# Kernel tuning notes

Measured on AMD Instinct MI355X. Metric: run time of the kernel, lower is better.

The kernel has to match this reference:

```python
import jax, jax.numpy as jnp
import numpy as np

EPS = 1e-5


def setup_inputs() -> dict:
    key = jax.random.key(0)
    ks = jax.random.split(key, 10)
    B, C, H, W = 8, 128, 64, 64
    inputs = jax.random.normal(ks[0], (B, C, H, W), dtype=jnp.float32)
    # GroupNorm affine params
    gn_w = jnp.ones((C,), dtype=jnp.float32)
    gn_b = jnp.zeros((C,), dtype=jnp.float32)
    # Linear layers: torch nn.Linear weight is [out, in]
    s = 1.0 / np.sqrt(C)
    Wq = jax.random.uniform(ks[1], (C, C), jnp.float32, -s, s)
    bq = jax.random.uniform(ks[2], (C,), jnp.float32, -s, s)
    Wk = jax.random.uniform(ks[3], (C, C), jnp.float32, -s, s)
    bk = jax.random.uniform(ks[4], (C,), jnp.float32, -s, s)
    Wv = jax.random.uniform(ks[5], (C, C), jnp.float32, -s, s)
    bv = jax.random.uniform(ks[6], (C,), jnp.float32, -s, s)
    Wp = jax.random.uniform(ks[7], (C, C), jnp.float32, -s, s)
    bp = jax.random.uniform(ks[8], (C,), jnp.float32, -s, s)
    return {"inputs": inputs, "gn_w": gn_w, "gn_b": gn_b,
            "Wq": Wq, "bq": bq, "Wk": Wk, "bk": bk,
            "Wv": Wv, "bv": bv, "Wp": Wp, "bp": bp,
            "groups": 32}


def _group_norm(x, w, b, groups):
    B, C, H, W = x.shape
    xg = x.reshape(B, groups, C // groups, H, W)
    mu = jnp.mean(xg, axis=(2, 3, 4), keepdims=True)
    var = jnp.var(xg, axis=(2, 3, 4), keepdims=True)
    xn = ((xg - mu) * jax.lax.rsqrt(var + EPS)).reshape(B, C, H, W)
    return xn * w[None, :, None, None] + b[None, :, None, None]


def reference(inputs, gn_w, gn_b, Wq, bq, Wk, bk, Wv, bv, Wp, bp, groups):
    B, C, H, W = inputs.shape
    scale = C ** (-0.5)
    normed = _group_norm(inputs, gn_w, gn_b, groups)  # [B,C,H,W]
    x = normed.transpose(0, 2, 3, 1).reshape(B, H * W, C)  # [B,N,C] tokens
    q = x @ Wq.T + bq
    k = x @ Wk.T + bk
    v = x @ Wv.T + bv
    # full dense attention over N = H*W tokens, single head
    scores = jnp.einsum('bnc,bmc->bnm', q, k) * scale  # [B,N,N]
    attn = jax.nn.softmax(scores, axis=-1)
    out = jnp.einsum('bnm,bmc->bnc', attn, v)
    proj = out @ Wp.T + bp
    proj = proj.reshape(B, H, W, C).transpose(0, 3, 1, 2)
    return normed + proj
```

## Files before the change

kernel.cpp:

```cpp
#include <hip/hip_runtime.h>
#include <hip/hip_bf16.h>
#include <math.h>

typedef __bf16 bf16_t;
typedef __bf16 bf16x8 __attribute__((ext_vector_type(8)));
typedef float  f32x4  __attribute__((ext_vector_type(4)));
typedef float  f32x16 __attribute__((ext_vector_type(16)));

#define BB 8
#define CC 128
#define NN 4096
#define LDP 136
#define SCALE2 0.12751743342f

static __device__ __forceinline__ f32x4 mfma16(bf16x8 a, bf16x8 b, f32x4 c) {
    return __builtin_amdgcn_mfma_f32_16x16x32_bf16(a, b, c, 0, 0, 0);
}
static __device__ __forceinline__ f32x16 mfma32(bf16x8 a, bf16x8 b, f32x16 c) {
    return __builtin_amdgcn_mfma_f32_32x32x16_bf16(a, b, c, 0, 0, 0);
}
static __device__ __forceinline__ void gld16(const void* g, void* l) {
    __builtin_amdgcn_global_load_lds(
        (const __attribute__((address_space(1))) void*)g,
        (__attribute__((address_space(3))) void*)l, 16, 0, 0);
}
static __device__ __forceinline__ unsigned pack2bf(float a, float b) {
    union { bf16_t h[2]; unsigned u; } r;
    r.h[0] = (bf16_t)a; r.h[1] = (bf16_t)b;
    return r.u;
}

__global__ void __launch_bounds__(1024) gn_stats(const float* __restrict__ in,
                                                 float* __restrict__ stats) {
    int bg = blockIdx.x;
    const float4* p4 = (const float4*)(in + (size_t)bg * 16384);
    int tid = threadIdx.x;
    float s = 0.f, ss = 0.f;
    for (int i = tid; i < 4096; i += 1024) {
        float4 v = p4[i];
        s  += v.x + v.y + v.z + v.w;
        ss += v.x*v.x + v.y*v.y + v.z*v.z + v.w*v.w;
    }
    for (int off = 1; off < 64; off <<= 1) {
        s  += __shfl_xor(s,  off, 64);
        ss += __shfl_xor(ss, off, 64);
    }
    __shared__ float red[32];
    int wv = tid >> 6;
    if ((tid & 63) == 0) { red[wv*2] = s; red[wv*2+1] = ss; }
    __syncthreads();
    if (tid == 0) {
        float S = 0.f, SS = 0.f;
        #pragma unroll
        for (int i = 0; i < 16; i++) { S += red[2*i]; SS += red[2*i+1]; }
        float mu  = S * (1.f/16384.f);
        float var = SS * (1.f/16384.f) - mu*mu;
        stats[bg*2]   = mu;
        stats[bg*2+1] = rsqrtf(var + 1e-5f);
    }
}

__global__ void __launch_bounds__(512) qkv_gemm(const float* __restrict__ in,
        const float* __restrict__ stats, const float* __restrict__ gw, const float* __restrict__ gb,
        const float* __restrict__ Wq, const float* __restrict__ bq,
        const float* __restrict__ Wk, const float* __restrict__ bk,
        const float* __restrict__ Wv, const float* __restrict__ bv,
        bf16_t* __restrict__ q, bf16_t* __restrict__ k, bf16_t* __restrict__ vT) {
    __shared__ bf16_t wb[CC * LDP];
    __shared__ bf16_t xt[128 * 130];
    int b  = blockIdx.x >> 5;
    int n0 = (blockIdx.x & 31) << 7;
    int tid = threadIdx.x;
    int lane = tid & 63, l15 = lane & 15, quad = lane >> 4;
    int w = tid >> 6;

    for (int i = tid; i < 4096; i += 512) {
        int c = i >> 5, p4 = i & 31;
        const float4* inp = (const float4*)(in + (size_t)(b*CC + c)*NN + n0);
        float4 v = inp[p4];
        int sg = b*32 + (c >> 2);
        float mu = stats[sg*2], rs = stats[sg*2+1];
        float gwc = gw[c], gbc = gb[c];
        xt[(p4*4 + 0)*130 + c] = (bf16_t)((v.x - mu)*rs*gwc + gbc);
        xt[(p4*4 + 1)*130 + c] = (bf16_t)((v.y - mu)*rs*gwc + gbc);
        xt[(p4*4 + 2)*130 + c] = (bf16_t)((v.z - mu)*rs*gwc + gbc);
        xt[(p4*4 + 3)*130 + c] = (bf16_t)((v.w - mu)*rs*gwc + gbc);
    }
    for (int i = tid; i < 2048; i += 512) {
        int row = i >> 4, s8 = i & 15;
        const float* wp = Wq + row*128 + s8*8;
        bf16x8 v;
        #pragma unroll
        for (int j = 0; j < 8; j++) v[j] = (bf16_t)wp[j];
        *(bf16x8*)&wb[row*LDP + s8*8] = v;
    }
    __syncthreads();
    bf16x8 afr[4];
    #pragma unroll
    for (int kb = 0; kb < 4; kb++)
        afr[kb] = *(const bf16x8*)&xt[(w*16 + l15)*130 + kb*32 + quad*8];

    for (int ph = 0; ph < 3; ph++) {
        const float* bs = (ph == 0) ? bq : (ph == 1 ? bk : bv);
        f32x4 acc[8];
        f32x4 z = {0.f, 0.f, 0.f, 0.f};
        #pragma unroll
        for (int t = 0; t < 8; t++) acc[t] = z;
        #pragma unroll
        for (int kb = 0; kb < 4; kb++)
            #pragma unroll
            for (int t = 0; t < 8; t++) {
                bf16x8 bf = *(const bf16x8*)&wb[(t*16 + l15)*LDP + kb*32 + quad*8];
                acc[t] = mfma16(afr[kb], bf, acc[t]);
            }
        __syncthreads();
        if (ph < 2) {
            float sc = (ph == 0) ? SCALE2 : 1.0f;
            #pragma unroll
            for (int t = 0; t < 8; t++) {
                float bias = bs[t*16 + l15];
                #pragma unroll
                for (int r = 0; r < 4; r++) {
                    int nloc = w*16 + quad*4 + r;
                    wb[nloc*LDP + t*16 + l15] = (bf16_t)((acc[t][r] + bias) * sc);
                }
            }
            __syncthreads();
            bf16_t* outp = (ph == 0) ? q : k;
            for (int i = tid; i < 2048; i += 512) {
                int row = i >> 4, g = i & 15;
                bf16x8 vv = *(const bf16x8*)&wb[row*LDP + g*8];
                int gd = (ph == 0) ? g : (g ^ (row & 15));
                *(bf16x8*)&outp[(size_t)(b*NN + n0 + row)*CC + gd*8] = vv;
            }
        } else {
            #pragma unroll
            for (int t = 0; t < 8; t++) {
                float bias = bs[t*16 + l15];
                #pragma unroll
                for (int r = 0; r < 4; r++) {
                    int nloc = w*16 + quad*4 + r;
                    wb[(t*16 + l15)*LDP + nloc] = (bf16_t)(acc[t][r] + bias);
                }
            }
            __syncthreads();
            for (int i = tid; i < 8192; i += 512) {
                int c = i >> 6, np = i & 63;
                unsigned int d = *(const unsigned int*)&wb[c*LDP + np*2];
                int npp = (np & ~6) | ((np & 2) << 1) | ((np & 4) >> 1);
                int g = (npp >> 2) ^ (c & 15);
                *(unsigned int*)&vT[(size_t)(b*CC + c)*NN + n0 + (g << 3) + ((npp & 3) << 1)] = d;
            }
        }
        if (ph < 2) {
            __syncthreads();
            const float* Wn = (ph == 0) ? Wk : Wv;
            for (int i = tid; i < 2048; i += 512) {
                int row = i >> 4, s8 = i & 15;
                const float* wp = Wn + row*128 + s8*8;
                bf16x8 v;
                #pragma unroll
                for (int j = 0; j < 8; j++) v[j] = (bf16_t)wp[j];
                *(bf16x8*)&wb[row*LDP + s8*8] = v;
            }
            __syncthreads();
        }
    }
}

__global__ void __launch_bounds__(512, 2) flash_attn(const bf16_t* __restrict__ qg_,
                                                     const bf16_t* __restrict__ kg,
                                                     const bf16_t* __restrict__ vg,
                                                     unsigned* __restrict__ opd,
                                                     float* __restrict__ mlf) {
    __shared__ bf16_t kbuf[2][128*128];
    __shared__ bf16_t vbuf[2][128*128];
    const int b    = blockIdx.x >> 5;
    const int qb   = (blockIdx.x >> 1) & 15;
    const int jh   = blockIdx.x & 1;
    const int q0   = qb << 8;
    const int j00  = jh << 11;
    const int tid  = threadIdx.x;
    const int lane = tid & 63;
    const int l31  = lane & 31;
    const int h    = lane >> 5;
    const int w    = tid >> 6;

    bf16x8 qf[8];
    {
        const bf16_t* qr = qg_ + ((size_t)(b*NN + q0 + w*32 + l31))*CC + h*8;
        #pragma unroll
        for (int kc = 0; kc < 8; kc++) qf[kc] = *(const bf16x8*)(qr + kc*16);
    }
    int gofs[8];
    #pragma unroll
    for (int kc = 0; kc < 8; kc++) gofs[kc] = ((2*kc + h) ^ (l31 & 15)) << 3;

    f32x16 ot[4];
    #pragma unroll
    for (int ct = 0; ct < 4; ct++)
        #pragma unroll
        for (int r = 0; r < 16; r++) ot[ct][r] = 0.f;
    float l = 0.f;

    {
        const bf16_t* kt = kg + ((size_t)(b*NN + j00))*CC;
        #pragma unroll
        for (int it = 0; it < 4; it++) {
            int cb = it*512 + tid;
            gld16(kt + (size_t)cb*8, &kbuf[0][cb*8]);
        }
        #pragma unroll
        for (int it = 0; it < 4; it++) {
            int c = it*512 + tid;
            gld16(vg + ((size_t)(b*CC + (c >> 4)))*NN + j00 + (c & 15)*8, &vbuf[0][c*8]);
        }
    }
    __syncthreads();

    for (int i = 0; i < 16; i++) {
        const int cur = i & 1;
        if (i < 15) {
            const int j0n = j00 + ((i + 1) << 7);
            const bf16_t* kt = kg + ((size_t)(b*NN + j0n))*CC;
            #pragma unroll
            for (int it = 0; it < 4; it++) {
                int cb = it*512 + tid;
                gld16(kt + (size_t)cb*8, &kbuf[cur^1][cb*8]);
            }
            #pragma unroll
            for (int it = 0; it < 4; it++) {
                int c = it*512 + tid;
                gld16(vg + ((size_t)(b*CC + (c >> 4)))*NN + j0n + (c & 15)*8, &vbuf[cur^1][c*8]);
            }
        }
        f32x16 st[4];
        #pragma unroll
        for (int tt = 0; tt < 4; tt++)
            #pragma unroll
            for (int r = 0; r < 16; r++) st[tt][r] = 0.f;
        #pragma unroll
        for (int kc = 0; kc < 8; kc++) {
            #pragma unroll
            for (int tt = 0; tt < 4; tt++) {
                bf16x8 kf = *(const bf16x8*)&kbuf[cur][(tt*32 + l31)*128 + gofs[kc]];
                st[tt] = mfma32(kf, qf[kc], st[tt]);
            }
        }
        #pragma unroll
        for (int tt = 0; tt < 4; tt++) {
            #pragma unroll
            for (int r = 0; r < 16; r++) st[tt][r] = __builtin_amdgcn_exp2f(st[tt][r]);
            {
                float a0 = (st[tt][0]+st[tt][1]) + (st[tt][2]+st[tt][3]);
                float a1 = (st[tt][4]+st[tt][5]) + (st[tt][6]+st[tt][7]);
                float a2 = (st[tt][8]+st[tt][9]) + (st[tt][10]+st[tt][11]);
                float a3 = (st[tt][12]+st[tt][13]) + (st[tt][14]+st[tt][15]);
                l += (a0 + a1) + (a2 + a3);
            }
            union { unsigned u[4]; bf16x8 v; } pf[2];
            #pragma unroll
            for (int kcl = 0; kcl < 2; kcl++)
                #pragma unroll
                for (int g = 0; g < 4; g++)
                    pf[kcl].u[g] = pack2bf(st[tt][8*kcl + 2*g], st[tt][8*kcl + 2*g + 1]);
            #pragma unroll
            for (int kcl = 0; kcl < 2; kcl++) {
                const int kc = tt*2 + kcl;
                #pragma unroll
                for (int ct = 0; ct < 4; ct++) {
                    bf16x8 vf = *(const bf16x8*)&vbuf[cur][(ct*32 + l31)*128 + gofs[kc]];
                    ot[ct] = mfma32(vf, pf[kcl].v, ot[ct]);
                }
            }
        }
        __syncthreads();
    }
    l += __shfl_xor(l, 32, 64);
    const int row0 = q0 + w*32 + l31;
    unsigned* ob = opd + ((size_t)(jh*BB + b)) * 64 * NN;
    #pragma unroll
    for (int ct = 0; ct < 4; ct++)
        #pragma unroll
        for (int rp = 0; rp < 8; rp++) {
            int cpair = ct*16 + (rp & 1) + 4*(rp >> 1) + 2*h;
            ob[(size_t)cpair*NN + row0] = pack2bf(ot[ct][2*rp], ot[ct][2*rp + 1]);
        }
    if (h == 0)
        mlf[((size_t)(jh*BB + b))*NN + row0] = l;
}

__global__ void __launch_bounds__(512) proj_out(const unsigned* __restrict__ opd,
                                                const float* __restrict__ mlf,
                                                const float* __restrict__ Wp,
                                                const float* __restrict__ bp,
                                                const float* __restrict__ in,
                                                const float* __restrict__ stats,
                                                const float* __restrict__ gw,
                                                const float* __restrict__ gb,
                                                float* __restrict__ out) {
    __shared__ bf16_t wb[CC * LDP];
    __shared__ bf16_t aot[128 * 130];
    __shared__ float invl[128];
    int b  = blockIdx.x >> 5;
    int n0 = (blockIdx.x & 31) << 7;
    int tid = threadIdx.x;
    int lane = tid & 63, l15 = lane & 15, quad = lane >> 4;
    int w = tid >> 6;
    if (tid < 128) {
        float lt = mlf[(size_t)b*NN + n0 + tid] + mlf[((size_t)(BB + b))*NN + n0 + tid];
        invl[tid] = 1.0f / lt;
    }
    for (int i = tid; i < 2048; i += 512) {
        int row = i >> 4, s8 = i & 15;
        const float* wp = Wp + row*128 + s8*8;
        bf16x8 v;
        #pragma unroll
        for (int j = 0; j < 8; j++) v[j] = (bf16_t)wp[j];
        *(bf16x8*)&wb[row*LDP + s8*8] = v;
    }
    __syncthreads();
    for (int i = tid; i < 8192; i += 512) {
        int qq = i & 127, cp = i >> 7;
        unsigned u0 = opd[((size_t)b*64 + cp)*NN + n0 + qq];
        unsigned u1 = opd[(((size_t)(BB + b))*64 + cp)*NN + n0 + qq];
        union { unsigned u; float f; } a0, c0, a1, c1;
        a0.u = u0 << 16; c0.u = u0 & 0xffff0000u;
        a1.u = u1 << 16; c1.u = u1 & 0xffff0000u;
        float s = invl[qq];
        *(unsigned*)&aot[qq*130 + cp*2] = pack2bf((a0.f + a1.f) * s, (c0.f + c1.f) * s);
    }
    __syncthreads();
    bf16x8 afr[4];
    #pragma unroll
    for (int kb = 0; kb < 4; kb++)
        afr[kb] = *(const bf16x8*)&aot[(w*16 + l15)*130 + kb*32 + quad*8];
    f32x4 acc[8];
    f32x4 z = {0.f, 0.f, 0.f, 0.f};
    #pragma unroll
    for (int t = 0; t < 8; t++) acc[t] = z;
    #pragma unroll
    for (int kb = 0; kb < 4; kb++)
        #pragma unroll
        for (int t = 0; t < 8; t++) {
            bf16x8 bf = *(const bf16x8*)&wb[(t*16 + l15)*LDP + kb*32 + quad*8];
            acc[t] = mfma16(afr[kb], bf, acc[t]);
        }
    __syncthreads();
    #pragma unroll
    for (int t = 0; t < 8; t++) {
        float bias = bp[t*16 + l15];
        #pragma unroll
        for (int r = 0; r < 4; r++) {
            int nloc = w*16 + quad*4 + r;
            wb[(t*16 + l15)*LDP + nloc] = (bf16_t)(acc[t][r] + bias);
        }
    }
    __syncthreads();
    for (int i = tid; i < 8192; i += 512) {
        int c = i >> 6, np = i & 63;
        bf16_t b0 = wb[c*LDP + np*2], b1 = wb[c*LDP + np*2 + 1];
        size_t idx = (size_t)(b*CC + c)*NN + n0 + np*2;
        int sg = b*32 + (c >> 2);
        float mu = stats[sg*2], rs = stats[sg*2+1];
        float gwc = gw[c], gbc = gb[c];
        float2 iv = *(const float2*)&in[idx];
        float2 ov;
        ov.x = (iv.x - mu)*rs*gwc + gbc + (float)b0;
        ov.y = (iv.y - mu)*rs*gwc + gbc + (float)b1;
        *(float2*)&out[idx] = ov;
    }
}

extern "C" void kernel_launch(void* const* d_in, const int* in_sizes, int n_in,
                              void* d_out, int out_size, void* d_ws, size_t ws_size,
                              hipStream_t stream) {
    const float* in = (const float*)d_in[0];
    const float* gw = (const float*)d_in[1];
    const float* gb = (const float*)d_in[2];
    const float* Wq = (const float*)d_in[3];
    const float* bq = (const float*)d_in[4];
    const float* Wk = (const float*)d_in[5];
    const float* bk = (const float*)d_in[6];
    const float* Wv = (const float*)d_in[7];
    const float* bv = (const float*)d_in[8];
    const float* Wp = (const float*)d_in[9];
    const float* bp = (const float*)d_in[10];
    float* out = (float*)d_out;

    char* ws = (char*)d_ws;
    const size_t SZ = (size_t)BB * NN * CC * 2;
    float*    stats = (float*)ws;
    bf16_t*   q  = (bf16_t*)(ws + 2048);
    bf16_t*   kk = (bf16_t*)(ws + 2048 + SZ);
    bf16_t*   vT = (bf16_t*)(ws + 2048 + 2*SZ);
    unsigned* op = (unsigned*)(ws + 2048 + 3*SZ);
    float*    ml = (float*)(ws + 2048 + 3*SZ + (size_t)2*BB*64*NN*4);

    gn_stats  <<<256, 1024, 0, stream>>>(in, stats);
    qkv_gemm  <<<256,  512, 0, stream>>>(in, stats, gw, gb, Wq, bq, Wk, bk, Wv, bv, q, kk, vT);
    flash_attn<<<256,  512, 0, stream>>>(q, kk, vT, op, ml);
    proj_out  <<<256,  512, 0, stream>>>(op, ml, Wp, bp, in, stats, gw, gb, out);
}
```

Before: 181.3 us.

## Split attention KV range four ways, single-buffer LDS, cache normalized input as bf16

```diff
diff --git a/kernel.cpp b/kernel.cpp
--- a/kernel.cpp
+++ b/kernel.cpp
@@ -65,7 +65,8 @@
         const float* __restrict__ Wq, const float* __restrict__ bq,
         const float* __restrict__ Wk, const float* __restrict__ bk,
         const float* __restrict__ Wv, const float* __restrict__ bv,
-        bf16_t* __restrict__ q, bf16_t* __restrict__ k, bf16_t* __restrict__ vT) {
+        bf16_t* __restrict__ q, bf16_t* __restrict__ k, bf16_t* __restrict__ vT,
+        bf16_t* __restrict__ xn) {
     __shared__ bf16_t wb[CC * LDP];
     __shared__ bf16_t xt[128 * 130];
     int b  = blockIdx.x >> 5;
@@ -81,10 +82,18 @@
         int sg = b*32 + (c >> 2);
         float mu = stats[sg*2], rs = stats[sg*2+1];
         float gwc = gw[c], gbc = gb[c];
-        xt[(p4*4 + 0)*130 + c] = (bf16_t)((v.x - mu)*rs*gwc + gbc);
-        xt[(p4*4 + 1)*130 + c] = (bf16_t)((v.y - mu)*rs*gwc + gbc);
-        xt[(p4*4 + 2)*130 + c] = (bf16_t)((v.z - mu)*rs*gwc + gbc);
-        xt[(p4*4 + 3)*130 + c] = (bf16_t)((v.w - mu)*rs*gwc + gbc);
+        float x0 = (v.x - mu)*rs*gwc + gbc;
+        float x1 = (v.y - mu)*rs*gwc + gbc;
+        float x2 = (v.z - mu)*rs*gwc + gbc;
+        float x3 = (v.w - mu)*rs*gwc + gbc;
+        xt[(p4*4 + 0)*130 + c] = (bf16_t)x0;
+        xt[(p4*4 + 1)*130 + c] = (bf16_t)x1;
+        xt[(p4*4 + 2)*130 + c] = (bf16_t)x2;
+        xt[(p4*4 + 3)*130 + c] = (bf16_t)x3;
+        uint2 pk;
+        pk.x = pack2bf(x0, x1);
+        pk.y = pack2bf(x2, x3);
+        *(uint2*)&xn[(size_t)(b*CC + c)*NN + n0 + p4*4] = pk;
     }
     for (int i = tid; i < 2048; i += 512) {
         int row = i >> 4, s8 = i & 15;
@@ -173,13 +182,13 @@
                                                      const bf16_t* __restrict__ vg,
                                                      unsigned* __restrict__ opd,
                                                      float* __restrict__ mlf) {
-    __shared__ bf16_t kbuf[2][128*128];
-    __shared__ bf16_t vbuf[2][128*128];
-    const int b    = blockIdx.x >> 5;
-    const int qb   = (blockIdx.x >> 1) & 15;
-    const int jh   = blockIdx.x & 1;
+    __shared__ bf16_t kbuf[128*128];
+    __shared__ bf16_t vbuf[128*128];
+    const int b    = blockIdx.x >> 6;
+    const int qb   = (blockIdx.x >> 2) & 15;
+    const int jq   = blockIdx.x & 3;
     const int q0   = qb << 8;
-    const int j00  = jh << 11;
+    const int j00  = jq << 10;
     const int tid  = threadIdx.x;
     const int lane = tid & 63;
     const int l31  = lane & 31;
@@ -208,32 +217,17 @@
         #pragma unroll
         for (int it = 0; it < 4; it++) {
             int cb = it*512 + tid;
-            gld16(kt + (size_t)cb*8, &kbuf[0][cb*8]);
+            gld16(kt + (size_t)cb*8, &kbuf[cb*8]);
         }
         #pragma unroll
         for (int it = 0; it < 4; it++) {
             int c = it*512 + tid;
-            gld16(vg + ((size_t)(b*CC + (c >> 4)))*NN + j00 + (c & 15)*8, &vbuf[0][c*8]);
-        }
-    }
-    __syncthreads();
-
-    for (int i = 0; i < 16; i++) {
-        const int cur = i & 1;
-        if (i < 15) {
-            const int j0n = j00 + ((i + 1) << 7);
-            const bf16_t* kt = kg + ((size_t)(b*NN + j0n))*CC;
-            #pragma unroll
-            for (int it = 0; it < 4; it++) {
-                int cb = it*512 + tid;
-                gld16(kt + (size_t)cb*8, &kbuf[cur^1][cb*8]);
-            }
-            #pragma unroll
-            for (int it = 0; it < 4; it++) {
-                int c = it*512 + tid;
-                gld16(vg + ((size_t)(b*CC + (c >> 4)))*NN + j0n + (c & 15)*8, &vbuf[cur^1][c*8]);
-            }
-        }
+            gld16(vg + ((size_t)(b*CC + (c >> 4)))*NN + j00 + (c & 15)*8, &vbuf[c*8]);
+        }
+    }
+    __syncthreads();
+
+    for (int i = 0; i < 8; i++) {
         f32x16 st[4];
         #pragma unroll
         for (int tt = 0; tt < 4; tt++)
@@ -243,7 +237,7 @@
         for (int kc = 0; kc < 8; kc++) {
             #pragma unroll
             for (int tt = 0; tt < 4; tt++) {
-                bf16x8 kf = *(const bf16x8*)&kbuf[cur][(tt*32 + l31)*128 + gofs[kc]];
+                bf16x8 kf = *(const bf16x8*)&kbuf[(tt*32 + l31)*128 + gofs[kc]];
                 st[tt] = mfma32(kf, qf[kc], st[tt]);
             }
         }
@@ -269,16 +263,31 @@
                 const int kc = tt*2 + kcl;
                 #pragma unroll
                 for (int ct = 0; ct < 4; ct++) {
-                    bf16x8 vf = *(const bf16x8*)&vbuf[cur][(ct*32 + l31)*128 + gofs[kc]];
+                    bf16x8 vf = *(const bf16x8*)&vbuf[(ct*32 + l31)*128 + gofs[kc]];
                     ot[ct] = mfma32(vf, pf[kcl].v, ot[ct]);
                 }
             }
         }
-        __syncthreads();
+        if (i < 7) {
+            __syncthreads();
+            const int j0n = j00 + ((i + 1) << 7);
+            const bf16_t* kt = kg + ((size_t)(b*NN + j0n))*CC;
+            #pragma unroll
+            for (int it = 0; it < 4; it++) {
+                int cb = it*512 + tid;
+                gld16(kt + (size_t)cb*8, &kbuf[cb*8]);
+            }
+            #pragma unroll
+            for (int it = 0; it < 4; it++) {
+                int c = it*512 + tid;
+                gld16(vg + ((size_t)(b*CC + (c >> 4)))*NN + j0n + (c & 15)*8, &vbuf[c*8]);
+            }
+            __syncthreads();
+        }
     }
     l += __shfl_xor(l, 32, 64);
     const int row0 = q0 + w*32 + l31;
-    unsigned* ob = opd + ((size_t)(jh*BB + b)) * 64 * NN;
+    unsigned* ob = opd + ((size_t)(jq*BB + b)) * 64 * NN;
     #pragma unroll
     for (int ct = 0; ct < 4; ct++)
         #pragma unroll
@@ -287,17 +296,14 @@
             ob[(size_t)cpair*NN + row0] = pack2bf(ot[ct][2*rp], ot[ct][2*rp + 1]);
         }
     if (h == 0)
-        mlf[((size_t)(jh*BB + b))*NN + row0] = l;
+        mlf[((size_t)(jq*BB + b))*NN + row0] = l;
 }
 
 __global__ void __launch_bounds__(512) proj_out(const unsigned* __restrict__ opd,
                                                 const float* __restrict__ mlf,
                                                 const float* __restrict__ Wp,
                                                 const float* __restrict__ bp,
-                                                const float* __restrict__ in,
-                                                const float* __restrict__ stats,
-                                                const float* __restrict__ gw,
-                                                const float* __restrict__ gb,
+                                                const bf16_t* __restrict__ xn,
                                                 float* __restrict__ out) {
     __shared__ bf16_t wb[CC * LDP];
     __shared__ bf16_t aot[128 * 130];
@@ -308,7 +314,9 @@
     int lane = tid & 63, l15 = lane & 15, quad = lane >> 4;
     int w = tid >> 6;
     if (tid < 128) {
-        float lt = mlf[(size_t)b*NN + n0 + tid] + mlf[((size_t)(BB + b))*NN + n0 + tid];
+        float lt = 0.f;
+        #pragma unroll
+        for (int p = 0; p < 4; p++) lt += mlf[((size_t)(p*BB + b))*NN + n0 + tid];
         invl[tid] = 1.0f / lt;
     }
     for (int i = tid; i < 2048; i += 512) {
@@ -322,13 +330,16 @@
     __syncthreads();
     for (int i = tid; i < 8192; i += 512) {
         int qq = i & 127, cp = i >> 7;
-        unsigned u0 = opd[((size_t)b*64 + cp)*NN + n0 + qq];
-        unsigned u1 = opd[(((size_t)(BB + b))*64 + cp)*NN + n0 + qq];
-        union { unsigned u; float f; } a0, c0, a1, c1;
-        a0.u = u0 << 16; c0.u = u0 & 0xffff0000u;
-        a1.u = u1 << 16; c1.u = u1 & 0xffff0000u;
+        float lo = 0.f, hi = 0.f;
+        #pragma unroll
+        for (int p = 0; p < 4; p++) {
+            unsigned u = opd[(((size_t)(p*BB + b))*64 + cp)*NN + n0 + qq];
+            union { unsigned u; float f; } a, c;
+            a.u = u << 16; c.u = u & 0xffff0000u;
+            lo += a.f; hi += c.f;
+        }
         float s = invl[qq];
-        *(unsigned*)&aot[qq*130 + cp*2] = pack2bf((a0.f + a1.f) * s, (c0.f + c1.f) * s);
+        *(unsigned*)&aot[qq*130 + cp*2] = pack2bf(lo * s, hi * s);
     }
     __syncthreads();
     bf16x8 afr[4];
@@ -361,13 +372,12 @@
         int c = i >> 6, np = i & 63;
         bf16_t b0 = wb[c*LDP + np*2], b1 = wb[c*LDP + np*2 + 1];
         size_t idx = (size_t)(b*CC + c)*NN + n0 + np*2;
-        int sg = b*32 + (c >> 2);
-        float mu = stats[sg*2], rs = stats[sg*2+1];
-        float gwc = gw[c], gbc = gb[c];
-        float2 iv = *(const float2*)&in[idx];
+        unsigned xu = *(const unsigned*)&xn[idx];
+        union { unsigned u; float f; } x0, x1;
+        x0.u = xu << 16; x1.u = xu & 0xffff0000u;
         float2 ov;
-        ov.x = (iv.x - mu)*rs*gwc + gbc + (float)b0;
-        ov.y = (iv.y - mu)*rs*gwc + gbc + (float)b1;
+        ov.x = x0.f + (float)b0;
+        ov.y = x1.f + (float)b1;
         *(float2*)&out[idx] = ov;
     }
 }
@@ -394,11 +404,12 @@
     bf16_t*   q  = (bf16_t*)(ws + 2048);
     bf16_t*   kk = (bf16_t*)(ws + 2048 + SZ);
     bf16_t*   vT = (bf16_t*)(ws + 2048 + 2*SZ);
-    unsigned* op = (unsigned*)(ws + 2048 + 3*SZ);
-    float*    ml = (float*)(ws + 2048 + 3*SZ + (size_t)2*BB*64*NN*4);
+    bf16_t*   xn = (bf16_t*)(ws + 2048 + 3*SZ);
+    unsigned* op = (unsigned*)(ws + 2048 + 4*SZ);
+    float*    ml = (float*)(ws + 2048 + 4*SZ + (size_t)4*BB*64*NN*4);
 
     gn_stats  <<<256, 1024, 0, stream>>>(in, stats);
-    qkv_gemm  <<<256,  512, 0, stream>>>(in, stats, gw, gb, Wq, bq, Wk, bk, Wv, bv, q, kk, vT);
-    flash_attn<<<256,  512, 0, stream>>>(q, kk, vT, op, ml);
-    proj_out  <<<256,  512, 0, stream>>>(op, ml, Wp, bp, in, stats, gw, gb, out);
-}
+    qkv_gemm  <<<256,  512, 0, stream>>>(in, stats, gw, gb, Wq, bq, Wk, bk, Wv, bv, q, kk, vT, xn);
+    flash_attn<<<512,  512, 0, stream>>>(q, kk, vT, op, ml);
+    proj_out  <<<256,  512, 0, stream>>>(op, ml, Wp, bp, xn, out);
+}
```

Result: slower. 185.3 us (+2.2%).

## Halve token tiles in QKV/proj kernels and reuse bf16 normalized activations

Applied to the files above, without the earlier changes.

```diff
diff --git a/kernel.cpp b/kernel.cpp
--- a/kernel.cpp
+++ b/kernel.cpp
@@ -60,33 +60,42 @@
     }
 }
 
-__global__ void __launch_bounds__(512) qkv_gemm(const float* __restrict__ in,
+__global__ void __launch_bounds__(256) qkv_gemm(const float* __restrict__ in,
         const float* __restrict__ stats, const float* __restrict__ gw, const float* __restrict__ gb,
         const float* __restrict__ Wq, const float* __restrict__ bq,
         const float* __restrict__ Wk, const float* __restrict__ bk,
         const float* __restrict__ Wv, const float* __restrict__ bv,
-        bf16_t* __restrict__ q, bf16_t* __restrict__ k, bf16_t* __restrict__ vT) {
+        bf16_t* __restrict__ q, bf16_t* __restrict__ k, bf16_t* __restrict__ vT,
+        bf16_t* __restrict__ xn) {
     __shared__ bf16_t wb[CC * LDP];
-    __shared__ bf16_t xt[128 * 130];
-    int b  = blockIdx.x >> 5;
-    int n0 = (blockIdx.x & 31) << 7;
+    __shared__ bf16_t xt[64 * 130];
+    int b  = blockIdx.x >> 6;
+    int n0 = (blockIdx.x & 63) << 6;
     int tid = threadIdx.x;
     int lane = tid & 63, l15 = lane & 15, quad = lane >> 4;
     int w = tid >> 6;
 
-    for (int i = tid; i < 4096; i += 512) {
-        int c = i >> 5, p4 = i & 31;
+    for (int i = tid; i < 2048; i += 256) {
+        int c = i >> 4, p4 = i & 15;
         const float4* inp = (const float4*)(in + (size_t)(b*CC + c)*NN + n0);
         float4 v = inp[p4];
         int sg = b*32 + (c >> 2);
         float mu = stats[sg*2], rs = stats[sg*2+1];
         float gwc = gw[c], gbc = gb[c];
-        xt[(p4*4 + 0)*130 + c] = (bf16_t)((v.x - mu)*rs*gwc + gbc);
-        xt[(p4*4 + 1)*130 + c] = (bf16_t)((v.y - mu)*rs*gwc + gbc);
-        xt[(p4*4 + 2)*130 + c] = (bf16_t)((v.z - mu)*rs*gwc + gbc);
-        xt[(p4*4 + 3)*130 + c] = (bf16_t)((v.w - mu)*rs*gwc + gbc);
-    }
-    for (int i = tid; i < 2048; i += 512) {
+        float x0 = (v.x - mu)*rs*gwc + gbc;
+        float x1 = (v.y - mu)*rs*gwc + gbc;
+        float x2 = (v.z - mu)*rs*gwc + gbc;
+        float x3 = (v.w - mu)*rs*gwc + gbc;
+        xt[(p4*4 + 0)*130 + c] = (bf16_t)x0;
+        xt[(p4*4 + 1)*130 + c] = (bf16_t)x1;
+        xt[(p4*4 + 2)*130 + c] = (bf16_t)x2;
+        xt[(p4*4 + 3)*130 + c] = (bf16_t)x3;
+        uint2 pk;
+        pk.x = pack2bf(x0, x1);
+        pk.y = pack2bf(x2, x3);
+        *(uint2*)&xn[(size_t)(b*CC + c)*NN + n0 + p4*4] = pk;
+    }
+    for (int i = tid; i < 2048; i += 256) {
         int row = i >> 4, s8 = i & 15;
         const float* wp = Wq + row*128 + s8*8;
         bf16x8 v;
@@ -127,7 +136,7 @@
             }
             __syncthreads();
             bf16_t* outp = (ph == 0) ? q : k;
-            for (int i = tid; i < 2048; i += 512) {
+            for (int i = tid; i < 1024; i += 256) {
                 int row = i >> 4, g = i & 15;
                 bf16x8 vv = *(const bf16x8*)&wb[row*LDP + g*8];
                 int gd = (ph == 0) ? g : (g ^ (row & 15));
@@ -144,18 +153,21 @@
                 }
             }
             __syncthreads();
-            for (int i = tid; i < 8192; i += 512) {
-                int c = i >> 6, np = i & 63;
+            int half8 = (n0 >> 3) & 8;
+            size_t nseg = n0 & ~127;
+            for (int i = tid; i < 4096; i += 256) {
+                int c = i >> 5, np = i & 31;
                 unsigned int d = *(const unsigned int*)&wb[c*LDP + np*2];
                 int npp = (np & ~6) | ((np & 2) << 1) | ((np & 4) >> 1);
-                int g = (npp >> 2) ^ (c & 15);
-                *(unsigned int*)&vT[(size_t)(b*CC + c)*NN + n0 + (g << 3) + ((npp & 3) << 1)] = d;
+                int g128 = (npp >> 2) + half8;
+                int gs = g128 ^ (c & 15);
+                *(unsigned int*)&vT[(size_t)(b*CC + c)*NN + nseg + (gs << 3) + ((npp & 3) << 1)] = d;
             }
         }
         if (ph < 2) {
             __syncthreads();
             const float* Wn = (ph == 0) ? Wk : Wv;
-            for (int i = tid; i < 2048; i += 512) {
+            for (int i = tid; i < 2048; i += 256) {
                 int row = i >> 4, s8 = i & 15;
                 const float* wp = Wn + row*128 + s8*8;
                 bf16x8 v;
@@ -290,28 +302,25 @@
         mlf[((size_t)(jh*BB + b))*NN + row0] = l;
 }
 
-__global__ void __launch_bounds__(512) proj_out(const unsigned* __restrict__ opd,
+__global__ void __launch_bounds__(256) proj_out(const unsigned* __restrict__ opd,
                                                 const float* __restrict__ mlf,
                                                 const float* __restrict__ Wp,
                                                 const float* __restrict__ bp,
-                                                const float* __restrict__ in,
-                                                const float* __restrict__ stats,
-                                                const float* __restrict__ gw,
-                                                const float* __restrict__ gb,
+                                                const bf16_t* __restrict__ xn,
                                                 float* __restrict__ out) {
     __shared__ bf16_t wb[CC * LDP];
-    __shared__ bf16_t aot[128 * 130];
-    __shared__ float invl[128];
-    int b  = blockIdx.x >> 5;
-    int n0 = (blockIdx.x & 31) << 7;
+    __shared__ bf16_t aot[64 * 130];
+    __shared__ float invl[64];
+    int b  = blockIdx.x >> 6;
+    int n0 = (blockIdx.x & 63) << 6;
     int tid = threadIdx.x;
     int lane = tid & 63, l15 = lane & 15, quad = lane >> 4;
     int w = tid >> 6;
-    if (tid < 128) {
+    if (tid < 64) {
         float lt = mlf[(size_t)b*NN + n0 + tid] + mlf[((size_t)(BB + b))*NN + n0 + tid];
         invl[tid] = 1.0f / lt;
     }
-    for (int i = tid; i < 2048; i += 512) {
+    for (int i = tid; i < 2048; i += 256) {
         int row = i >> 4, s8 = i & 15;
         const float* wp = Wp + row*128 + s8*8;
         bf16x8 v;
@@ -320,8 +329,8 @@
         *(bf16x8*)&wb[row*LDP + s8*8] = v;
     }
     __syncthreads();
-    for (int i = tid; i < 8192; i += 512) {
-        int qq = i & 127, cp = i >> 7;
+    for (int i = tid; i < 4096; i += 256) {
+        int qq = i & 63, cp = i >> 6;
         unsigned u0 = opd[((size_t)b*64 + cp)*NN + n0 + qq];
         unsigned u1 = opd[(((size_t)(BB + b))*64 + cp)*NN + n0 + qq];
         union { unsigned u; float f; } a0, c0, a1, c1;
@@ -357,17 +366,16 @@
         }
     }
     __syncthreads();
-    for (int i = tid; i < 8192; i += 512) {
-        int c = i >> 6, np = i & 63;
+    for (int i = tid; i < 4096; i += 256) {
+        int c = i >> 5, np = i & 31;
         bf16_t b0 = wb[c*LDP + np*2], b1 = wb[c*LDP + np*2 + 1];
         size_t idx = (size_t)(b*CC + c)*NN + n0 + np*2;
-        int sg = b*32 + (c >> 2);
-        float mu = stats[sg*2], rs = stats[sg*2+1];
-        float gwc = gw[c], gbc = gb[c];
-        float2 iv = *(const float2*)&in[idx];
+        unsigned xu = *(const unsigned*)&xn[idx];
+        union { unsigned u; float f; } x0, x1;
+        x0.u = xu << 16; x1.u = xu & 0xffff0000u;
         float2 ov;
-        ov.x = (iv.x - mu)*rs*gwc + gbc + (float)b0;
-        ov.y = (iv.y - mu)*rs*gwc + gbc + (float)b1;
+        ov.x = x0.f + (float)b0;
+        ov.y = x1.f + (float)b1;
         *(float2*)&out[idx] = ov;
     }
 }
@@ -394,11 +402,12 @@
     bf16_t*   q  = (bf16_t*)(ws + 2048);
     bf16_t*   kk = (bf16_t*)(ws + 2048 + SZ);
     bf16_t*   vT = (bf16_t*)(ws + 2048 + 2*SZ);
-    unsigned* op = (unsigned*)(ws + 2048 + 3*SZ);
-    float*    ml = (float*)(ws + 2048 + 3*SZ + (size_t)2*BB*64*NN*4);
+    bf16_t*   xn = (bf16_t*)(ws + 2048 + 3*SZ);
+    unsigned* op = (unsigned*)(ws + 2048 + 4*SZ);
+    float*    ml = (float*)(ws + 2048 + 4*SZ + (size_t)2*BB*64*NN*4);
 
     gn_stats  <<<256, 1024, 0, stream>>>(in, stats);
-    qkv_gemm  <<<256,  512, 0, stream>>>(in, stats, gw, gb, Wq, bq, Wk, bk, Wv, bv, q, kk, vT);
+    qkv_gemm  <<<512,  256, 0, stream>>>(in, stats, gw, gb, Wq, bq, Wk, bk, Wv, bv, q, kk, vT, xn);
     flash_attn<<<256,  512, 0, stream>>>(q, kk, vT, op, ml);
-    proj_out  <<<256,  512, 0, stream>>>(op, ml, Wp, bp, in, stats, gw, gb, out);
-}
+    proj_out  <<<512,  256, 0, stream>>>(op, ml, Wp, bp, xn, out);
+}
```

Measured after the change: 181.4 us, median of 2. No clear change (+0.1%).
